# Kernel tuning notes

Hardware: AMD Instinct MI355X
Metric: run time of the kernel (lower is better)

## Reference

```python
import jax, jax.numpy as jnp
import numpy as np

NEG_SLOPE = 0.2


def setup_inputs() -> dict:
    key = jax.random.key(0)
    ks = jax.random.split(key, 7)
    N, E, IN, H, D = 100000, 1000000, 256, 4, 32
    feat = jax.random.normal(ks[0], (N, IN), dtype=jnp.float32)
    W_fc = jax.random.normal(ks[1], (H * D, IN), dtype=jnp.float32) * (1.0 / np.sqrt(IN))
    attn_l = jax.random.normal(ks[2], (1, H, D), dtype=jnp.float32) * 0.1
    attn_r = jax.random.normal(ks[3], (1, H, D), dtype=jnp.float32) * 0.1
    bias = jnp.zeros((H * D,), dtype=jnp.float32)
    src = jax.random.randint(ks[4], (E,), 0, N, dtype=jnp.int32)
    dst = jax.random.randint(ks[5], (E,), 0, N, dtype=jnp.int32)
    return {"feat": feat, "W_fc": W_fc, "attn_l": attn_l, "attn_r": attn_r, "bias": bias, "src": src, "dst": dst}


def reference(feat, W_fc, attn_l, attn_r, bias, src, dst):
    N = feat.shape[0]
    H, D = attn_l.shape[1], attn_l.shape[2]
    # fc projection; note: in the non-tuple path the module uses self.fc for
    # BOTH feat_src and feat_src2, so they are identical.
    h = (feat @ W_fc.T).reshape(N, H, D)  # [N,H,D]
    el = jnp.sum(h * attn_l, axis=-1)  # [N,H]
    er = jnpp_sum = jnp.sum(h * attn_r, axis=-1)  # [N,H]
    e = jax.nn.leaky_relu(el[src] + er[dst], NEG_SLOPE)  # [E,H]
    # edge softmax normalized over incoming edges of each dst node
    e_max = jax.ops.segment_max(e, dst, num_segments=N)  # [N,H]
    ex = jnp.exp(e - e_max[dst])
    denom = jax.ops.segment_sum(ex, dst, num_segments=N)  # [N,H]
    a = ex / denom[dst]  # [E,H]
    # attention-weighted aggregation: sum_e a_e * h[src_e] -> dst
    initial_ft = jax.ops.segment_sum(h[src] * a[:, :, None], dst, num_segments=N)
    # second path: u_mul_v then sum to dst (feat_src2 == feat_dst2 == h)
    add_ft = jax.ops.segment_sum(h[src] * h[dst], dst, num_segments=N)
    rst = initial_ft + add_ft + bias.reshape(1, H, D)
    return rst
```

## Files before the change

### kernel.cpp

```cpp
#include <hip/hip_runtime.h>
#include <hip/hip_bf16.h>
#include <hip/hip_fp16.h>
#include <math.h>

#define NEG_SLOPE 0.2f

typedef __attribute__((ext_vector_type(8))) short short8v;
typedef __attribute__((ext_vector_type(4))) float f32x4;

__device__ __forceinline__ float uas(unsigned int u) { return __uint_as_float(u); }

__device__ __forceinline__ unsigned short f2bf(float x) {
    __hip_bfloat16 b = __float2bfloat16(x);
    return *(unsigned short*)&b;
}

#define NPB_SHIFT 8
#define BIN_EPT   16
#define BIN_EDGES (256 * BIN_EPT)

__global__ void k_prep(const float* __restrict__ W, const float* __restrict__ al,
                       const float* __restrict__ ar, short* __restrict__ wfrag,
                       int* __restrict__ bcount, int NB) {
    int p = blockIdx.x * 256 + threadIdx.x;
    if (p < NB) bcount[p] = 0;
    if (p >= 144 * 32) return;
    int n = p >> 5, kg = p & 31;
    float v[8];
    if (n < 128) {
        const float* wp = W + (size_t)n * 256 + kg * 8;
        float4 v0 = *(const float4*)wp;
        float4 v1 = *(const float4*)(wp + 4);
        v[0] = v0.x; v[1] = v0.y; v[2] = v0.z; v[3] = v0.w;
        v[4] = v1.x; v[5] = v1.y; v[6] = v1.z; v[7] = v1.w;
    } else if (n < 136) {
        int i = n - 128, hh = i & 3, lr = i >> 2;
        const float* av = lr ? ar : al;
#pragma unroll
        for (int j = 0; j < 8; j++) v[j] = 0.f;
        for (int c = 0; c < 32; c++) {
            float a = av[hh * 32 + c];
            const float* wp = W + (size_t)(hh * 32 + c) * 256 + kg * 8;
#pragma unroll
            for (int j = 0; j < 8; j++) v[j] += a * wp[j];
        }
    } else {
#pragma unroll
        for (int j = 0; j < 8; j++) v[j] = 0.f;
    }
    short s8[8];
#pragma unroll
    for (int j = 0; j < 8; j++) s8[j] = (short)f2bf(v[j]);
    int kstep = kg >> 2, ntile = n >> 4;
    int L     = (kg & 3) * 16 + (n & 15);
    int slot  = kstep * 9 + ntile;
    *(short8v*)&wfrag[(slot * 64 + L) * 8] = *(short8v*)s8;
}

__global__ __launch_bounds__(256) void k_gemm(const float* __restrict__ feat,
                                              const short* __restrict__ wfrag,
                                              unsigned short* __restrict__ hb,
                                              float* __restrict__ el,
                                              float* __restrict__ er, int N,
                                              const int* __restrict__ dst,
                                              int* __restrict__ bcount,
                                              int E, int NB) {
    __shared__ short wlds[32768];
    __shared__ int bh[512];
    const int t    = threadIdx.x;
    const int lane = t & 63;
    const int wave = t >> 6;
    const int n0   = blockIdx.x * 64;
    const int g    = lane >> 4;
    const int c    = lane & 15;
    const bool do_hist = (blockIdx.x * BIN_EDGES) < E;

    if (do_hist) {
        for (int i = t; i < 512; i += 256) bh[i] = 0;
    }

#pragma unroll
    for (int i = 0; i < 16; i++) {
        int p  = t + i * 256;
        int sl = p >> 6, li = p & 63;
        int gs = (sl >> 3) * 9 + (sl & 7);
        *(short8v*)&wlds[(size_t)p * 8] =
            *(const short8v*)&wfrag[((size_t)gs * 64 + li) * 8];
    }

    const int row = n0 + wave * 16 + c;
    const int rc  = row < N ? row : N - 1;
    const float* ap = feat + (size_t)rc * 256 + g * 8;
    float4 a4[16];
#pragma unroll
    for (int ks = 0; ks < 8; ks++) {
        a4[2 * ks]     = *(const float4*)(ap + ks * 32);
        a4[2 * ks + 1] = *(const float4*)(ap + ks * 32 + 4);
    }

    __syncthreads();

    f32x4 acc[9];
#pragma unroll
    for (int nt = 0; nt < 9; nt++) acc[nt] = (f32x4){0.f, 0.f, 0.f, 0.f};

#pragma unroll
    for (int ks = 0; ks < 8; ks++) {
        float4 v0 = a4[2 * ks], v1 = a4[2 * ks + 1];
        short s8[8];
        s8[0] = (short)f2bf(v0.x); s8[1] = (short)f2bf(v0.y);
        s8[2] = (short)f2bf(v0.z); s8[3] = (short)f2bf(v0.w);
        s8[4] = (short)f2bf(v1.x); s8[5] = (short)f2bf(v1.y);
        s8[6] = (short)f2bf(v1.z); s8[7] = (short)f2bf(v1.w);
        short8v afrag = *(short8v*)s8;
        short8v b8 = *(const short8v*)&wfrag[(((size_t)ks * 9 + 8) * 64 + lane) * 8];
#pragma unroll
        for (int nt = 0; nt < 8; nt++) {
            short8v b = *(short8v*)&wlds[(((size_t)ks * 8 + nt) * 64 + lane) * 8];
            acc[nt] = __builtin_amdgcn_mfma_f32_16x16x32_bf16(afrag, b, acc[nt], 0, 0, 0);
        }
        acc[8] = __builtin_amdgcn_mfma_f32_16x16x32_bf16(afrag, b8, acc[8], 0, 0, 0);
    }

#pragma unroll
    for (int r = 0; r < 4; r++) {
        int m = n0 + wave * 16 + g * 4 + r;
        if (m < N) {
#pragma unroll
            for (int nt = 0; nt < 8; nt++)
                hb[(size_t)m * 128 + nt * 16 + c] = f2bf(acc[nt][r]);
            float av = acc[8][r];
            if (c < 4)      el[(size_t)m * 4 + c]       = av;
            else if (c < 8) er[(size_t)m * 4 + (c - 4)] = av;
        }
    }

    if (do_hist) {
        int base = blockIdx.x * BIN_EDGES + t;
#pragma unroll
        for (int k = 0; k < BIN_EPT; k++) {
            int idx = base + k * 256;
            if (idx < E) atomicAdd(&bh[dst[idx] >> NPB_SHIFT], 1);
        }
        __syncthreads();
        for (int i = t; i < NB; i += 256) {
            int h = bh[i];
            if (h) atomicAdd(&bcount[i], h);
        }
    }
}

__global__ __launch_bounds__(512) void k_bscan(const int* __restrict__ bcount,
                                               int* __restrict__ bbase,
                                               int* __restrict__ bcur, int NB) {
    __shared__ int s[512];
    int t = threadIdx.x;
    int h = (t < NB) ? bcount[t] : 0;
    s[t] = h;
    __syncthreads();
    for (int off = 1; off < 512; off <<= 1) {
        int v = (t >= off) ? s[t - off] : 0;
        __syncthreads();
        s[t] += v;
        __syncthreads();
    }
    int excl = s[t] - h;
    if (t <= NB) bbase[t] = excl;
    if (t < NB)  bcur[t]  = excl;
}

__global__ __launch_bounds__(256) void k_binscatter(const int* __restrict__ src,
                                                    const int* __restrict__ dst,
                                                    int* __restrict__ bcur,
                                                    unsigned int* __restrict__ binned,
                                                    int E, int NB) {
    __shared__ int hist[512];
    __shared__ int cur[512];
    int t = threadIdx.x;
    for (int i = t; i < NB; i += 256) hist[i] = 0;
    __syncthreads();
    int base = blockIdx.x * BIN_EDGES + t;
    int sv[BIN_EPT], dv[BIN_EPT];
#pragma unroll
    for (int k = 0; k < BIN_EPT; k++) {
        int idx = base + k * 256;
        if (idx < E) {
            sv[k] = src[idx];
            dv[k] = dst[idx];
            atomicAdd(&hist[dv[k] >> NPB_SHIFT], 1);
        } else {
            dv[k] = -1;
        }
    }
    __syncthreads();
    for (int i = t; i < NB; i += 256) {
        int h = hist[i];
        cur[i] = h ? atomicAdd(&bcur[i], h) : 0;
    }
    __syncthreads();
#pragma unroll
    for (int k = 0; k < BIN_EPT; k++) {
        if (dv[k] >= 0) {
            int p = atomicAdd(&cur[dv[k] >> NPB_SHIFT], 1);
            binned[p] = (unsigned int)sv[k] | ((unsigned int)(dv[k] & 255) << 24);
        }
    }
}

__global__ __launch_bounds__(256) void k_csr(const unsigned int* __restrict__ binned,
                                             const int* __restrict__ bbase,
                                             int* __restrict__ startA,
                                             int* __restrict__ deg,
                                             int* __restrict__ src_csr, int N) {
    __shared__ int hist[256];
    __shared__ int scn[256];
    __shared__ int cur[256];
    int b = blockIdx.x;
    int t = threadIdx.x;
    int base = bbase[b];
    int cnt  = bbase[b + 1] - base;
    int node0 = b << NPB_SHIFT;
    hist[t] = 0;
    __syncthreads();
    for (int i = t; i < cnt; i += 256) {
        unsigned int e = binned[base + i];
        atomicAdd(&hist[e >> 24], 1);
    }
    __syncthreads();
    int h = hist[t];
    scn[t] = h;
    __syncthreads();
    for (int off = 1; off < 256; off <<= 1) {
        int v = (t >= off) ? scn[t - off] : 0;
        __syncthreads();
        scn[t] += v;
        __syncthreads();
    }
    int excl  = scn[t] - h;
    int gnode = node0 + t;
    if (gnode < N) { deg[gnode] = h; startA[gnode] = base + excl; }
    cur[t] = excl;
    __syncthreads();
    for (int i = t; i < cnt; i += 256) {
        unsigned int e = binned[base + i];
        int p = atomicAdd(&cur[e >> 24], 1);
        src_csr[base + p] = (int)(e & 0xFFFFFFu);
    }
}

__global__ __launch_bounds__(256) void k_agg(
        const unsigned int* __restrict__ hbu,
        const float* __restrict__ el, const float* __restrict__ er,
        const int* __restrict__ src_csr,
        const int* __restrict__ start, const int* __restrict__ deg,
        const float* __restrict__ bias, float* __restrict__ out, int N) {
    int wid  = blockIdx.x * 4 + (threadIdx.x >> 6);
    int lane = threadIdx.x & 63;
    if (wid >= N) return;
    int beg = __builtin_amdgcn_readfirstlane(start[wid]);
    int dg  = __builtin_amdgcn_readfirstlane(deg[wid]);
    int head = lane >> 4;

    float er_own = er[(size_t)wid * 4 + head];

    float S1x = 0.f, S1y = 0.f, S2x = 0.f, S2y = 0.f, dd = 0.f;
    int i = 0;
    for (; i + 4 <= dg; i += 4) {
        int b = beg + i;
        int s0 = src_csr[b], s1 = src_csr[b + 1], s2 = src_csr[b + 2], s3 = src_csr[b + 3];
        unsigned int u0 = hbu[(size_t)s0 * 64 + lane];
        unsigned int u1 = hbu[(size_t)s1 * 64 + lane];
        unsigned int u2 = hbu[(size_t)s2 * 64 + lane];
        unsigned int u3 = hbu[(size_t)s3 * 64 + lane];
        float t0 = el[(size_t)s0 * 4 + head] + er_own;
        float t1 = el[(size_t)s1 * 4 + head] + er_own;
        float t2 = el[(size_t)s2 * 4 + head] + er_own;
        float t3 = el[(size_t)s3 * 4 + head] + er_own;
        t0 = t0 > 0.f ? t0 : NEG_SLOPE * t0;
        t1 = t1 > 0.f ? t1 : NEG_SLOPE * t1;
        t2 = t2 > 0.f ? t2 : NEG_SLOPE * t2;
        t3 = t3 > 0.f ? t3 : NEG_SLOPE * t3;
        float w0 = __expf(t0), w1 = __expf(t1), w2 = __expf(t2), w3 = __expf(t3);
        float x0 = uas(u0 << 16), y0 = uas(u0 & 0xFFFF0000u);
        float x1 = uas(u1 << 16), y1 = uas(u1 & 0xFFFF0000u);
        float x2 = uas(u2 << 16), y2 = uas(u2 & 0xFFFF0000u);
        float x3 = uas(u3 << 16), y3 = uas(u3 & 0xFFFF0000u);
        S1x += (x0 + x1) + (x2 + x3);
        S1y += (y0 + y1) + (y2 + y3);
        S2x += w0 * x0 + w1 * x1 + w2 * x2 + w3 * x3;
        S2y += w0 * y0 + w1 * y1 + w2 * y2 + w3 * y3;
        dd  += (w0 + w1) + (w2 + w3);
    }
    for (; i < dg; i++) {
        int b = beg + i;
        int s0 = src_csr[b];
        unsigned int u0 = hbu[(size_t)s0 * 64 + lane];
        float t0 = el[(size_t)s0 * 4 + head] + er_own;
        t0 = t0 > 0.f ? t0 : NEG_SLOPE * t0;
        float w0 = __expf(t0);
        float x0 = uas(u0 << 16), y0 = uas(u0 & 0xFFFF0000u);
        S1x += x0; S1y += y0;
        S2x += w0 * x0; S2y += w0 * y0;
        dd  += w0;
    }

    unsigned int uh = hbu[(size_t)wid * 64 + lane];
    float hvx = uas(uh << 16), hvy = uas(uh & 0xFFFF0000u);
    float2 bv = ((const float2*)bias)[lane];
    float inv = dd > 0.f ? 1.f / dd : 0.f;
    float ox = bv.x + hvx * S1x + S2x * inv;
    float oy = bv.y + hvy * S1y + S2y * inv;
    float2 o = {ox, oy};
    ((float2*)(out + (size_t)wid * 128))[lane] = o;
}

extern "C" void kernel_launch(void* const* d_in, const int* in_sizes, int n_in,
                              void* d_out, int out_size, void* d_ws, size_t ws_size,
                              hipStream_t stream) {
    const float* feat = (const float*)d_in[0];
    const float* W_fc = (const float*)d_in[1];
    const float* al   = (const float*)d_in[2];
    const float* ar   = (const float*)d_in[3];
    const float* bias = (const float*)d_in[4];
    const int*   src  = (const int*)d_in[5];
    const int*   dst  = (const int*)d_in[6];
    const int N = in_sizes[0] / 256;
    const int E = in_sizes[5];
    const int NB = (N + 255) >> NPB_SHIFT;

    char* ws = (char*)d_ws;
    size_t off = 0;
    unsigned int* hbu = (unsigned int*)(ws + off); off += (size_t)N * 64 * 4;
    float* el         = (float*)(ws + off); off += (size_t)N * 4 * 4;
    float* er         = (float*)(ws + off); off += (size_t)N * 4 * 4;
    int* deg          = (int*)(ws + off);   off += (size_t)N * 4;
    int* startA       = (int*)(ws + off);   off += (size_t)N * 4;
    int* src_csr      = (int*)(ws + off);   off += (size_t)E * 4;
    unsigned int* binned = (unsigned int*)(ws + off); off += (size_t)E * 4;
    short* wfrag      = (short*)(ws + off); off += (size_t)72 * 64 * 8 * 2;
    int* bcount       = (int*)(ws + off);   off += 2048;
    int* bbase        = (int*)(ws + off);   off += 2064;
    int* bcur         = (int*)(ws + off);   off += 2048;

    float* out = (float*)d_out;

    k_prep<<<18, 256, 0, stream>>>(W_fc, al, ar, wfrag, bcount, NB);
    k_gemm<<<(N + 63) / 64, 256, 0, stream>>>(feat, wfrag, (unsigned short*)hbu,
                                              el, er, N, dst, bcount, E, NB);
    int binWG = (E + BIN_EDGES - 1) / BIN_EDGES;
    k_bscan<<<1, 512, 0, stream>>>(bcount, bbase, bcur, NB);
    k_binscatter<<<binWG, 256, 0, stream>>>(src, dst, bcur, binned, E, NB);
    k_csr<<<NB, 256, 0, stream>>>(binned, bbase, startA, deg, src_csr, N);
    k_agg<<<(N + 3) / 4, 256, 0, stream>>>(hbu, el, er, src_csr, startA, deg,
                                           bias, out, N);
}
```

Before: 273.7 us.

## Stage binning and CSR scatter in LDS, drop deg array, unroll aggregation by 8

The bin-scatter kernel now sorts each block's edges locally in shared memory by bucket and then writes them out contiguously, which makes the global writes coalesced instead of scattered. The CSR kernel stages each bucket's reordered sources in LDS before a coalesced copy, falling back to the old path when a bucket holds more than 3072 edges. The deg array is replaced by a start[N] sentinel written by the scan kernel, and the aggregation loop is unrolled to 8 edges so more gathers are in flight. The added shared-memory buffers (about 40 KB per block in binscatter) may lower occupancy.

```diff
diff --git a/kernel.cpp b/kernel.cpp
--- a/kernel.cpp
+++ b/kernel.cpp
@@ -152,7 +152,9 @@
 
 __global__ __launch_bounds__(512) void k_bscan(const int* __restrict__ bcount,
                                                int* __restrict__ bbase,
-                                               int* __restrict__ bcur, int NB) {
+                                               int* __restrict__ bcur,
+                                               int* __restrict__ startA,
+                                               int NB, int N) {
     __shared__ int s[512];
     int t = threadIdx.x;
     int h = (t < NB) ? bcount[t] : 0;
@@ -167,6 +169,7 @@
     int excl = s[t] - h;
     if (t <= NB) bbase[t] = excl;
     if (t < NB)  bcur[t]  = excl;
+    if (t == 0)  startA[N] = s[511];
 }
 
 __global__ __launch_bounds__(256) void k_binscatter(const int* __restrict__ src,
@@ -175,11 +178,17 @@
                                                     unsigned int* __restrict__ binned,
                                                     int E, int NB) {
     __shared__ int hist[512];
-    __shared__ int cur[512];
+    __shared__ int scn[512];
+    __shared__ int lcur[512];
+    __shared__ int gdelta[512];
+    __shared__ int ebuf[BIN_EDGES];
+    __shared__ int dbuf[BIN_EDGES];
     int t = threadIdx.x;
-    for (int i = t; i < NB; i += 256) hist[i] = 0;
-    __syncthreads();
-    int base = blockIdx.x * BIN_EDGES + t;
+    for (int i = t; i < 512; i += 256) hist[i] = 0;
+    __syncthreads();
+    int wbase = blockIdx.x * BIN_EDGES;
+    int base  = wbase + t;
+    int ne    = E - wbase; if (ne > BIN_EDGES) ne = BIN_EDGES;
     int sv[BIN_EPT], dv[BIN_EPT];
 #pragma unroll
     for (int k = 0; k < BIN_EPT; k++) {
@@ -193,28 +202,48 @@
         }
     }
     __syncthreads();
+    scn[t] = hist[t]; scn[t + 256] = hist[t + 256];
+    __syncthreads();
+    for (int off = 1; off < 512; off <<= 1) {
+        int a0 = (t >= off) ? scn[t - off] : 0;
+        int a1 = (t + 256 >= off) ? scn[t + 256 - off] : 0;
+        __syncthreads();
+        scn[t] += a0; scn[t + 256] += a1;
+        __syncthreads();
+    }
     for (int i = t; i < NB; i += 256) {
-        int h = hist[i];
-        cur[i] = h ? atomicAdd(&bcur[i], h) : 0;
+        int h  = hist[i];
+        int lb = scn[i] - h;
+        int g  = h ? atomicAdd(&bcur[i], h) : 0;
+        gdelta[i] = g - lb;
+        lcur[i]   = lb;
     }
     __syncthreads();
 #pragma unroll
     for (int k = 0; k < BIN_EPT; k++) {
         if (dv[k] >= 0) {
-            int p = atomicAdd(&cur[dv[k] >> NPB_SHIFT], 1);
-            binned[p] = (unsigned int)sv[k] | ((unsigned int)(dv[k] & 255) << 24);
-        }
+            int bkt  = dv[k] >> NPB_SHIFT;
+            int slot = atomicAdd(&lcur[bkt], 1);
+            ebuf[slot] = sv[k];
+            dbuf[slot] = dv[k];
+        }
+    }
+    __syncthreads();
+    for (int j = t; j < ne; j += 256) {
+        int d = dbuf[j];
+        binned[j + gdelta[d >> NPB_SHIFT]] =
+            (unsigned int)ebuf[j] | ((unsigned int)(d & 255) << 24);
     }
 }
 
 __global__ __launch_bounds__(256) void k_csr(const unsigned int* __restrict__ binned,
                                              const int* __restrict__ bbase,
                                              int* __restrict__ startA,
-                                             int* __restrict__ deg,
                                              int* __restrict__ src_csr, int N) {
     __shared__ int hist[256];
     __shared__ int scn[256];
     __shared__ int cur[256];
+    __shared__ int sbuf[3072];
     int b = blockIdx.x;
     int t = threadIdx.x;
     int base = bbase[b];
@@ -238,75 +267,103 @@
     }
     int excl  = scn[t] - h;
     int gnode = node0 + t;
-    if (gnode < N) { deg[gnode] = h; startA[gnode] = base + excl; }
+    if (gnode < N) startA[gnode] = base + excl;
     cur[t] = excl;
     __syncthreads();
-    for (int i = t; i < cnt; i += 256) {
-        unsigned int e = binned[base + i];
-        int p = atomicAdd(&cur[e >> 24], 1);
-        src_csr[base + p] = (int)(e & 0xFFFFFFu);
+    if (cnt <= 3072) {
+        for (int i = t; i < cnt; i += 256) {
+            unsigned int e = binned[base + i];
+            int p = atomicAdd(&cur[e >> 24], 1);
+            sbuf[p] = (int)(e & 0xFFFFFFu);
+        }
+        __syncthreads();
+        for (int i = t; i < cnt; i += 256)
+            src_csr[base + i] = sbuf[i];
+    } else {
+        for (int i = t; i < cnt; i += 256) {
+            unsigned int e = binned[base + i];
+            int p = atomicAdd(&cur[e >> 24], 1);
+            src_csr[base + p] = (int)(e & 0xFFFFFFu);
+        }
     }
 }
 
 __global__ __launch_bounds__(256) void k_agg(
         const unsigned int* __restrict__ hbu,
         const float* __restrict__ el, const float* __restrict__ er,
-        const int* __restrict__ src_csr,
-        const int* __restrict__ start, const int* __restrict__ deg,
+        const int* __restrict__ src_csr, const int* __restrict__ start,
         const float* __restrict__ bias, float* __restrict__ out, int N) {
     int wid  = blockIdx.x * 4 + (threadIdx.x >> 6);
     int lane = threadIdx.x & 63;
     if (wid >= N) return;
     int beg = __builtin_amdgcn_readfirstlane(start[wid]);
-    int dg  = __builtin_amdgcn_readfirstlane(deg[wid]);
+    int end = __builtin_amdgcn_readfirstlane(start[wid + 1]);
+    int dg  = end - beg;
     int head = lane >> 4;
 
     float er_own = er[(size_t)wid * 4 + head];
+    unsigned int uh = hbu[(size_t)wid * 64 + lane];
+    float2 bv = ((const float2*)bias)[lane];
 
     float S1x = 0.f, S1y = 0.f, S2x = 0.f, S2y = 0.f, dd = 0.f;
     int i = 0;
+    for (; i + 8 <= dg; i += 8) {
+        int b = beg + i;
+        int s[8];
+#pragma unroll
+        for (int k = 0; k < 8; k++) s[k] = src_csr[b + k];
+        unsigned int u[8];
+#pragma unroll
+        for (int k = 0; k < 8; k++) u[k] = hbu[(size_t)s[k] * 64 + lane];
+        float ev[8];
+#pragma unroll
+        for (int k = 0; k < 8; k++) ev[k] = el[(size_t)s[k] * 4 + head];
+#pragma unroll
+        for (int k = 0; k < 8; k++) {
+            float tt = ev[k] + er_own;
+            tt = fmaxf(tt, NEG_SLOPE * tt);
+            float w = __expf(tt);
+            float x = uas(u[k] << 16), y = uas(u[k] & 0xFFFF0000u);
+            S1x += x; S1y += y;
+            S2x += w * x; S2y += w * y;
+            dd  += w;
+        }
+    }
     for (; i + 4 <= dg; i += 4) {
         int b = beg + i;
-        int s0 = src_csr[b], s1 = src_csr[b + 1], s2 = src_csr[b + 2], s3 = src_csr[b + 3];
+        int s[4];
+#pragma unroll
+        for (int k = 0; k < 4; k++) s[k] = src_csr[b + k];
+        unsigned int u[4];
+#pragma unroll
+        for (int k = 0; k < 4; k++) u[k] = hbu[(size_t)s[k] * 64 + lane];
+        float ev[4];
+#pragma unroll
+        for (int k = 0; k < 4; k++) ev[k] = el[(size_t)s[k] * 4 + head];
+#pragma unroll
+        for (int k = 0; k < 4; k++) {
+            float tt = ev[k] + er_own;
+            tt = fmaxf(tt, NEG_SLOPE * tt);
+            float w = __expf(tt);
+            float x = uas(u[k] << 16), y = uas(u[k] & 0xFFFF0000u);
+            S1x += x; S1y += y;
+            S2x += w * x; S2y += w * y;
+            dd  += w;
+        }
+    }
+    for (; i < dg; i++) {
+        int s0 = src_csr[beg + i];
         unsigned int u0 = hbu[(size_t)s0 * 64 + lane];
-        unsigned int u1 = hbu[(size_t)s1 * 64 + lane];
-        unsigned int u2 = hbu[(size_t)s2 * 64 + lane];
-        unsigned int u3 = hbu[(size_t)s3 * 64 + lane];
-        float t0 = el[(size_t)s0 * 4 + head] + er_own;
-        float t1 = el[(size_t)s1 * 4 + head] + er_own;
-        float t2 = el[(size_t)s2 * 4 + head] + er_own;
-        float t3 = el[(size_t)s3 * 4 + head] + er_own;
-        t0 = t0 > 0.f ? t0 : NEG_SLOPE * t0;
-        t1 = t1 > 0.f ? t1 : NEG_SLOPE * t1;
-        t2 = t2 > 0.f ? t2 : NEG_SLOPE * t2;
-        t3 = t3 > 0.f ? t3 : NEG_SLOPE * t3;
-        float w0 = __expf(t0), w1 = __expf(t1), w2 = __expf(t2), w3 = __expf(t3);
-        float x0 = uas(u0 << 16), y0 = uas(u0 & 0xFFFF0000u);
-        float x1 = uas(u1 << 16), y1 = uas(u1 & 0xFFFF0000u);
-        float x2 = uas(u2 << 16), y2 = uas(u2 & 0xFFFF0000u);
-        float x3 = uas(u3 << 16), y3 = uas(u3 & 0xFFFF0000u);
-        S1x += (x0 + x1) + (x2 + x3);
-        S1y += (y0 + y1) + (y2 + y3);
-        S2x += w0 * x0 + w1 * x1 + w2 * x2 + w3 * x3;
-        S2y += w0 * y0 + w1 * y1 + w2 * y2 + w3 * y3;
-        dd  += (w0 + w1) + (w2 + w3);
-    }
-    for (; i < dg; i++) {
-        int b = beg + i;
-        int s0 = src_csr[b];
-        unsigned int u0 = hbu[(size_t)s0 * 64 + lane];
-        float t0 = el[(size_t)s0 * 4 + head] + er_own;
-        t0 = t0 > 0.f ? t0 : NEG_SLOPE * t0;
-        float w0 = __expf(t0);
+        float tt = el[(size_t)s0 * 4 + head] + er_own;
+        tt = fmaxf(tt, NEG_SLOPE * tt);
+        float w0 = __expf(tt);
         float x0 = uas(u0 << 16), y0 = uas(u0 & 0xFFFF0000u);
         S1x += x0; S1y += y0;
         S2x += w0 * x0; S2y += w0 * y0;
         dd  += w0;
     }
 
-    unsigned int uh = hbu[(size_t)wid * 64 + lane];
     float hvx = uas(uh << 16), hvy = uas(uh & 0xFFFF0000u);
-    float2 bv = ((const float2*)bias)[lane];
     float inv = dd > 0.f ? 1.f / dd : 0.f;
     float ox = bv.x + hvx * S1x + S2x * inv;
     float oy = bv.y + hvy * S1y + S2y * inv;
@@ -333,8 +390,7 @@
     unsigned int* hbu = (unsigned int*)(ws + off); off += (size_t)N * 64 * 4;
     float* el         = (float*)(ws + off); off += (size_t)N * 4 * 4;
     float* er         = (float*)(ws + off); off += (size_t)N * 4 * 4;
-    int* deg          = (int*)(ws + off);   off += (size_t)N * 4;
-    int* startA       = (int*)(ws + off);   off += (size_t)N * 4;
+    int* startA       = (int*)(ws + off);   off += (size_t)(N + 1) * 4;
     int* src_csr      = (int*)(ws + off);   off += (size_t)E * 4;
     unsigned int* binned = (unsigned int*)(ws + off); off += (size_t)E * 4;
     short* wfrag      = (short*)(ws + off); off += (size_t)72 * 64 * 8 * 2;
@@ -348,9 +404,9 @@
     k_gemm<<<(N + 63) / 64, 256, 0, stream>>>(feat, wfrag, (unsigned short*)hbu,
                                               el, er, N, dst, bcount, E, NB);
     int binWG = (E + BIN_EDGES - 1) / BIN_EDGES;
-    k_bscan<<<1, 512, 0, stream>>>(bcount, bbase, bcur, NB);
+    k_bscan<<<1, 512, 0, stream>>>(bcount, bbase, bcur, startA, NB, N);
     k_binscatter<<<binWG, 256, 0, stream>>>(src, dst, bcur, binned, E, NB);
-    k_csr<<<NB, 256, 0, stream>>>(binned, bbase, startA, deg, src_csr, N);
-    k_agg<<<(N + 3) / 4, 256, 0, stream>>>(hbu, el, er, src_csr, startA, deg,
+    k_csr<<<NB, 256, 0, stream>>>(binned, bbase, startA, src_csr, N);
+    k_agg<<<(N + 3) / 4, 256, 0, stream>>>(hbu, el, er, src_csr, startA,
                                            bias, out, N);
 }
```

Result: no change. 273.3 us (-0.2%).
